# Kernel tuning notes

Measured on AMD Instinct MI355X. Metric: run time of the kernel, lower is better.

The kernel has to match this reference:

```python
import jax, jax.numpy as jnp
import numpy as np

NUM_HEADS = 8
EPS = 1e-12  # torch F.normalize default eps


def setup_inputs() -> dict:
    key = jax.random.key(0)
    k0, k1, k2, k3 = jax.random.split(key, 4)
    b, c, d, h, w = 2, 64, 8, 128, 128
    x = jax.random.normal(k0, (b, c, d, h, w), dtype=jnp.float32)
    # 1x1x1 conv weights stored as [out, in]; depthwise 3x3x3 as [out, 1, kd, kh, kw]
    w_qkv = jax.random.normal(k1, (3 * c, c), dtype=jnp.float32) * 0.05
    w_dw = jax.random.normal(k2, (3 * c, 1, 3, 3, 3), dtype=jnp.float32) * 0.05
    temperature = jnp.ones((NUM_HEADS, 1, 1), dtype=jnp.float32)
    w_proj = jax.random.normal(k3, (c, c), dtype=jnp.float32) * 0.05
    return {"x": x, "w_qkv": w_qkv, "w_dw": w_dw, "temperature": temperature, "w_proj": w_proj}


def _l2norm(t):
    # F.normalize(t, dim=-1): t / max(||t||, eps)
    n = jnp.sqrt(jnp.sum(t * t, axis=-1, keepdims=True))
    return t / jnp.maximum(n, EPS)


def reference(x, w_qkv, w_dw, temperature, w_proj):
    b, c, d, h, w = x.shape
    heads = NUM_HEADS
    ch = c // heads  # per-head channel dim
    # 1x1x1 conv (pointwise) -> einsum over channels
    qkv = jnp.einsum('bcdhw,oc->bodhw', x, w_qkv)
    # depthwise 3x3x3 conv, padding 1 (SAME), groups = 3*c
    qkv = jax.lax.conv_general_dilated(
        qkv, w_dw, window_strides=(1, 1, 1), padding=[(1, 1)] * 3,
        feature_group_count=3 * c,
        dimension_numbers=('NCDHW', 'OIDHW', 'NCDHW'))
    q, k, v = jnp.split(qkv, 3, axis=1)
    n = d * h * w
    q = q.reshape(b, heads, ch, n)
    k = k.reshape(b, heads, ch, n)
    v = v.reshape(b, heads, ch, n)
    q = _l2norm(q)
    k = _l2norm(k)
    # channel-channel attention: [b, heads, ch, ch]
    attn = jnp.einsum('bhcn,bhen->bhce', q, k) * temperature
    attn = jax.nn.softmax(attn, axis=-1)
    out = jnp.einsum('bhce,bhen->bhcn', attn, v)
    out = out.reshape(b, c, d, h, w)
    out = jnp.einsum('bcdhw,oc->bodhw', out, w_proj)
    return out
```

## Files before the change

### kernel.cpp

```cpp
#include <hip/hip_runtime.h>
#include <math.h>

#define NPOS 131072
#define GC 128

typedef __attribute__((ext_vector_type(8))) short short8v;
typedef __attribute__((ext_vector_type(4))) float f32x4;

__device__ __forceinline__ void bf16split(float x, unsigned short& hi, unsigned short& lo) {
  unsigned u = __float_as_uint(x);
  hi = (unsigned short)(u >> 16);
  float hif = __uint_as_float(u & 0xffff0000u);
  float l = x - hif;
  lo = (unsigned short)(__float_as_uint(l) >> 16);
}

__global__ void k_prep(const float* __restrict__ w_qkv, unsigned short* __restrict__ whi,
                       unsigned short* __restrict__ wlo) {
  int idx = blockIdx.x * 256 + threadIdx.x;
  if (idx < 12288) {
    int j = idx & 7, l = (idx >> 3) & 63, ks = (idx >> 9) & 1, ot = (idx >> 10) & 3,
        g = idx >> 12;
    int out = ot * 16 + (l & 15);
    int k = ks * 32 + (l >> 4) * 8 + j;
    bf16split(w_qkv[(g * 64 + out) * 64 + k], whi[idx], wlo[idx]);
  }
}

__global__ __launch_bounds__(256) void k_pw_mfma(const float* __restrict__ x,
                                                 const unsigned short* __restrict__ whi,
                                                 const unsigned short* __restrict__ wlo,
                                                 float* __restrict__ pre) {
  const int b = blockIdx.y;
  const int lane = threadIdx.x & 63;
  const int wid = threadIdx.x >> 6;
  const int p0 = blockIdx.x * 256 + wid * 64;
  short8v ahi[4][2], alo[4][2];
#pragma unroll
  for (int ot = 0; ot < 4; ++ot)
#pragma unroll
    for (int ks = 0; ks < 2; ++ks) {
      int fi = ((ot * 2 + ks) * 64 + lane) * 8;
      ahi[ot][ks] = *(const short8v*)&whi[fi];
      alo[ot][ks] = *(const short8v*)&wlo[fi];
    }
  const int prow = lane & 15, kgrp = lane >> 4;
  const float* xb = x + ((size_t)b * 64 + kgrp * 8) * NPOS;
#pragma unroll
  for (int pt = 0; pt < 4; ++pt) {
    const int p = p0 + pt * 16 + prow;
    float xv[16];
#pragma unroll
    for (int ks = 0; ks < 2; ++ks)
#pragma unroll
      for (int j = 0; j < 8; ++j)
        xv[ks * 8 + j] = xb[(size_t)(ks * 32 + j) * NPOS + p];
    short8v bh[2], bl[2];
#pragma unroll
    for (int ks = 0; ks < 2; ++ks)
#pragma unroll
      for (int j = 0; j < 8; ++j) {
        unsigned short h, lo16;
        bf16split(xv[ks * 8 + j], h, lo16);
        bh[ks][j] = (short)h;
        bl[ks][j] = (short)lo16;
      }
#pragma unroll
    for (int ot = 0; ot < 4; ++ot) {
      f32x4 D = {0.f, 0.f, 0.f, 0.f};
#pragma unroll
      for (int ks = 0; ks < 2; ++ks) {
        D = __builtin_amdgcn_mfma_f32_16x16x32_bf16(ahi[ot][ks], bh[ks], D, 0, 0, 0);
        D = __builtin_amdgcn_mfma_f32_16x16x32_bf16(ahi[ot][ks], bl[ks], D, 0, 0, 0);
        D = __builtin_amdgcn_mfma_f32_16x16x32_bf16(alo[ot][ks], bh[ks], D, 0, 0, 0);
      }
      float* ob = pre + ((size_t)b * 64 + ot * 16 + kgrp * 4) * NPOS + p;
#pragma unroll
      for (int jj = 0; jj < 4; ++jj) ob[(size_t)jj * NPOS] = D[jj];
    }
  }
}

__device__ __forceinline__ void stage_tile(float (*t)[10][40], const float* __restrict__ in,
                                           int h0, int w0, int tid) {
  for (int i = tid; i < 800; i += 256) {
    int j = i & 7, row = i >> 3;
    int h = row % 10, dpl = row / 10;
    int dd = dpl - 1, hh = h0 + h - 1;
    float4 v = make_float4(0.f, 0.f, 0.f, 0.f);
    if (dd >= 0 && dd < 8 && hh >= 0 && hh < 128)
      v = *(const float4*)&in[((size_t)dd * 128 + hh) * 128 + (w0 + j * 4)];
    *(float4*)&t[dpl][h][4 + j * 4] = v;
  }
  for (int i = tid; i < 200; i += 256) {
    int side = i & 1, row = i >> 1;
    int h = row % 10, dpl = row / 10;
    int dd = dpl - 1, hh = h0 + h - 1;
    int ww = side ? (w0 + 32) : (w0 - 1);
    float v = 0.f;
    if (dd >= 0 && dd < 8 && hh >= 0 && hh < 128 && ww >= 0 && ww < 128)
      v = in[((size_t)dd * 128 + hh) * 128 + ww];
    t[dpl][h][side ? 36 : 3] = v;
  }
}

__device__ __forceinline__ void conv_droll(const float (*t)[10][40], const float* wk,
                                           int hl, int wl, float* acc) {
#pragma unroll
  for (int d = 0; d < 8; ++d) acc[d] = 0.f;
#pragma unroll
  for (int dpl = 0; dpl < 10; ++dpl) {
#pragma unroll
    for (int kh = 0; kh < 3; ++kh) {
#pragma unroll
      for (int kw = 0; kw < 3; ++kw) {
        float f = t[dpl][hl + kh][3 + wl + kw];
#pragma unroll
        for (int kd = 0; kd < 3; ++kd) {
          const int d = dpl - kd;
          if (d >= 0 && d < 8)
            acc[d] = fmaf(f, wk[(kd * 3 + kh) * 3 + kw], acc[d]);
        }
      }
    }
  }
}

__global__ __launch_bounds__(256) void k_dw(const float* __restrict__ pre,
                                            const float* __restrict__ w_dw,
                                            float* __restrict__ conv,
                                            float* __restrict__ nsq, int g) {
  const int id = blockIdx.x;
  const int sid = (id & 7) * 1024 + (id >> 3);
  const int z = sid >> 6, r = sid & 63, by = r >> 2, bx = r & 3;
  const int b = z >> 6;
  const int c = z & 63;
  const int h0 = by * 8;
  const int w0 = bx * 32;
  __shared__ float t[10][10][40];
  __shared__ float red[4];
  const int tid = threadIdx.y * 32 + threadIdx.x;
  stage_tile(t, pre + ((size_t)b * 64 + c) * NPOS, h0, w0, tid);
  float wk[27];
#pragma unroll
  for (int i = 0; i < 27; ++i) wk[i] = w_dw[(g * 64 + c) * 27 + i];
  __syncthreads();
  const int wl = threadIdx.x, hl = threadIdx.y;
  float acc[8];
  conv_droll(t, wk, hl, wl, acc);
  float* outp = conv + ((size_t)b * 64 + c) * NPOS + (size_t)(h0 + hl) * 128 + (w0 + wl);
  float nsum = 0.f;
#pragma unroll
  for (int d = 0; d < 8; ++d) {
    outp[(size_t)d * 16384] = acc[d];
    nsum = fmaf(acc[d], acc[d], nsum);
  }
  if (nsq) {
    const int lane = tid & 63, wv = tid >> 6;
    float v = nsum;
    v += __shfl_down(v, 32); v += __shfl_down(v, 16); v += __shfl_down(v, 8);
    v += __shfl_down(v, 4);  v += __shfl_down(v, 2);  v += __shfl_down(v, 1);
    if (lane == 0) red[wv] = v;
    __syncthreads();
    if (tid == 0) {
      const int blk = by * 4 + bx;
      nsq[((size_t)b * 64 + c) * 64 + blk] = red[0] + red[1] + red[2] + red[3];
    }
  }
}

__global__ __launch_bounds__(256) void k_gramS(const float* __restrict__ qconv,
                                               const float* __restrict__ kconv,
                                               float* __restrict__ partialS) {
  const int chunk = blockIdx.x;
  const int bh = blockIdx.y;
  const int b = bh >> 3, head = bh & 7;
  const int tid = threadIdx.x;
  const size_t base = ((size_t)b * 64 + head * 8) * NPOS + (size_t)chunk * 1024 + tid;
  const float* qb = qconv + base;
  const float* kb = kconv + base;
  float S[64];
#pragma unroll
  for (int i = 0; i < 64; ++i) S[i] = 0.f;
#pragma unroll
  for (int it = 0; it < 4; ++it) {
    const size_t off = (size_t)it * 256;
    float qv[8], kv[8];
#pragma unroll
    for (int c = 0; c < 8; ++c) qv[c] = qb[(size_t)c * NPOS + off];
#pragma unroll
    for (int e = 0; e < 8; ++e) kv[e] = kb[(size_t)e * NPOS + off];
#pragma unroll
    for (int c = 0; c < 8; ++c)
#pragma unroll
      for (int e = 0; e < 8; ++e) S[c * 8 + e] = fmaf(qv[c], kv[e], S[c * 8 + e]);
  }
#pragma unroll
  for (int i = 0; i < 64; ++i) asm volatile("" : "+v"(S[i]));

  const int lane = tid & 63, wv = tid >> 6;
#define BSTEP(src, dst, n, s)                                        \
  {                                                                  \
    const bool hi_ = (lane >> (s)) & 1;                              \
    _Pragma("unroll")                                                \
    for (int i_ = 0; i_ < (n); ++i_) {                               \
      float send_ = hi_ ? src[i_] : src[i_ + (n)];                   \
      float mine_ = hi_ ? src[i_ + (n)] : src[i_];                   \
      dst[i_] = mine_ + __shfl_xor(send_, 1 << (s));                 \
    }                                                                \
  }
  float v32[32], v16[16], v8[8], v4[4], v2[2], v1[1];
  BSTEP(S,   v32, 32, 0)
  BSTEP(v32, v16, 16, 1)
  BSTEP(v16, v8,   8, 2)
  BSTEP(v8,  v4,   4, 3)
  BSTEP(v4,  v2,   2, 4)
  BSTEP(v2,  v1,   1, 5)
#undef BSTEP
  const int idx = ((lane & 1) << 5) | ((lane & 2) << 3) | ((lane & 4) << 1) |
                  ((lane & 8) >> 1) | ((lane & 16) >> 3) | ((lane & 32) >> 5);
  __shared__ float red[4][64];
  red[wv][idx] = v1[0];
  __syncthreads();
  if (tid < 64) {
    float s = red[0][tid] + red[1][tid] + red[2][tid] + red[3][tid];
    partialS[((size_t)bh * GC + chunk) * 64 + tid] = s;
  }
}

__global__ void k_attn(const float* __restrict__ partialS, const float* __restrict__ nqp,
                       const float* __restrict__ nkp, const float* __restrict__ temp,
                       float* __restrict__ A) {
  const int bh = blockIdx.x;
  const int b = bh >> 3, head = bh & 7;
  const int tid = threadIdx.x;
  __shared__ float sums[80];
  if (tid < 64) {
    float s = 0.f;
    const float* pp = partialS + (size_t)bh * GC * 64 + tid;
    for (int j = 0; j < GC; ++j) s += pp[j * 64];
    sums[tid] = s;
  } else if (tid < 72) {
    const int e = tid - 64;
    float s = 0.f;
    const float* pp = nkp + ((size_t)b * 64 + head * 8 + e) * 64;
    for (int j = 0; j < 64; ++j) s += pp[j];
    sums[64 + e] = s;
  } else if (tid < 80) {
    const int c = tid - 72;
    float s = 0.f;
    const float* pp = nqp + ((size_t)b * 64 + head * 8 + c) * 64;
    for (int j = 0; j < 64; ++j) s += pp[j];
    sums[72 + c] = s;
  }
  __syncthreads();
  if (tid < 8) {
    const int c = tid;
    float tp = temp[head];
    float qd = fmaxf(sqrtf(sums[72 + c]), 1e-12f);
    float vals[8];
    float mx = -1e30f;
#pragma unroll
    for (int e = 0; e < 8; ++e) {
      float kd = fmaxf(sqrtf(sums[64 + e]), 1e-12f);
      vals[e] = sums[c * 8 + e] / (qd * kd) * tp;
      mx = fmaxf(mx, vals[e]);
    }
    float den = 0.f;
#pragma unroll
    for (int e = 0; e < 8; ++e) { vals[e] = expf(vals[e] - mx); den += vals[e]; }
#pragma unroll
    for (int e = 0; e < 8; ++e) A[bh * 64 + c * 8 + e] = vals[e] / den;
  }
}

__global__ void k_M(const float* __restrict__ w_proj, const float* __restrict__ A,
                    unsigned short* __restrict__ Mhi, unsigned short* __restrict__ Mlo) {
  const int b = blockIdx.x;
  for (int e = threadIdx.x; e < 4096; e += 256) {
    int j = e & 7, l = (e >> 3) & 63, ks = (e >> 9) & 1, ot = (e >> 10) & 3;
    int out = ot * 16 + (l & 15);
    int gch = ks * 32 + (l >> 4) * 8 + j;
    int hg = gch >> 3, jj = gch & 7;
    float s = 0.f;
#pragma unroll
    for (int i = 0; i < 8; ++i)
      s += w_proj[out * 64 + hg * 8 + i] * A[(b * 8 + hg) * 64 + i * 8 + jj];
    bf16split(s, Mhi[b * 4096 + e], Mlo[b * 4096 + e]);
  }
}

__global__ __launch_bounds__(256) void k_out_mfma(const float* __restrict__ vconv,
                                                  const unsigned short* __restrict__ Mhi,
                                                  const unsigned short* __restrict__ Mlo,
                                                  float* __restrict__ out) {
  const int b = blockIdx.y;
  const int lane = threadIdx.x & 63;
  const int wid = threadIdx.x >> 6;
  const int p0 = blockIdx.x * 256 + wid * 64;
  short8v ahi[4][2], alo[4][2];
#pragma unroll
  for (int ot = 0; ot < 4; ++ot)
#pragma unroll
    for (int ks = 0; ks < 2; ++ks) {
      int fi = b * 4096 + ((ot * 2 + ks) * 64 + lane) * 8;
      ahi[ot][ks] = *(const short8v*)&Mhi[fi];
      alo[ot][ks] = *(const short8v*)&Mlo[fi];
    }
  const int prow = lane & 15, kgrp = lane >> 4;
  const float* vb = vconv + ((size_t)b * 64 + kgrp * 8) * NPOS;
#pragma unroll
  for (int pt = 0; pt < 4; ++pt) {
    const int p = p0 + pt * 16 + prow;
    float xv[16];
#pragma unroll
    for (int ks = 0; ks < 2; ++ks)
#pragma unroll
      for (int j = 0; j < 8; ++j)
        xv[ks * 8 + j] = vb[(size_t)(ks * 32 + j) * NPOS + p];
    short8v bh[2], bl[2];
#pragma unroll
    for (int ks = 0; ks < 2; ++ks)
#pragma unroll
      for (int j = 0; j < 8; ++j) {
        unsigned short h, lo16;
        bf16split(xv[ks * 8 + j], h, lo16);
        bh[ks][j] = (short)h;
        bl[ks][j] = (short)lo16;
      }
#pragma unroll
    for (int ot = 0; ot < 4; ++ot) {
      f32x4 D = {0.f, 0.f, 0.f, 0.f};
#pragma unroll
      for (int ks = 0; ks < 2; ++ks) {
        D = __builtin_amdgcn_mfma_f32_16x16x32_bf16(ahi[ot][ks], bh[ks], D, 0, 0, 0);
        D = __builtin_amdgcn_mfma_f32_16x16x32_bf16(ahi[ot][ks], bl[ks], D, 0, 0, 0);
        D = __builtin_amdgcn_mfma_f32_16x16x32_bf16(alo[ot][ks], bh[ks], D, 0, 0, 0);
      }
      float* ob = out + ((size_t)b * 64 + ot * 16 + kgrp * 4) * NPOS + p;
#pragma unroll
      for (int jj = 0; jj < 4; ++jj) ob[(size_t)jj * NPOS] = D[jj];
    }
  }
}

extern "C" void kernel_launch(void* const* d_in, const int* in_sizes, int n_in,
                              void* d_out, int out_size, void* d_ws, size_t ws_size,
                              hipStream_t stream) {
  const float* x      = (const float*)d_in[0];
  const float* w_qkv  = (const float*)d_in[1];
  const float* w_dw   = (const float*)d_in[2];
  const float* temp   = (const float*)d_in[3];
  const float* w_proj = (const float*)d_in[4];
  float* out = (float*)d_out;
  float* ws  = (float*)d_ws;

  float* conv_buf = ws;
  float* kconv    = conv_buf + 16777216ull;
  float* nqp      = kconv + 16777216ull;
  float* nkp      = nqp + 8192ull;
  float* partialS = nkp + 8192ull;
  float* Abuf     = partialS + 131072ull;
  unsigned short* whi = (unsigned short*)(Abuf + 1024ull);
  unsigned short* wlo = whi + 12288ull;
  unsigned short* Mhi = wlo + 12288ull;
  unsigned short* Mlo = Mhi + 8192ull;

  k_prep<<<48, 256, 0, stream>>>(w_qkv, whi, wlo);
  k_pw_mfma<<<dim3(512, 2), 256, 0, stream>>>(x, whi, wlo, out);
  k_dw<<<8192, dim3(32, 8), 0, stream>>>(out, w_dw, conv_buf, nqp, 0);
  k_pw_mfma<<<dim3(512, 2), 256, 0, stream>>>(x, whi + 4096, wlo + 4096, out);
  k_dw<<<8192, dim3(32, 8), 0, stream>>>(out, w_dw, kconv, nkp, 1);
  k_gramS<<<dim3(GC, 16), 256, 0, stream>>>(conv_buf, kconv, partialS);
  k_attn<<<16, 128, 0, stream>>>(partialS, nqp, nkp, temp, Abuf);
  k_M<<<2, 256, 0, stream>>>(w_proj, Abuf, Mhi, Mlo);
  k_pw_mfma<<<dim3(512, 2), 256, 0, stream>>>(x, whi + 8192, wlo + 8192, out);
  k_dw<<<8192, dim3(32, 8), 0, stream>>>(out, w_dw, conv_buf, nullptr, 2);
  k_out_mfma<<<dim3(512, 2), 256, 0, stream>>>(conv_buf, Mhi, Mlo, out);
}
```

Measured before the change: 235.1 us.

## Stage pointwise-conv input tiles in LDS and split output channels across waves

The pointwise MFMA kernels now load a 64-channel by 64-position input tile into shared memory with coalesced float4 reads. Each of the four waves then computes one 16-row output-channel tile instead of all four. The old version had each wave read its own positions with strided scalar loads. The grid grows fourfold to match. This reduces per-wave weight registers and improves load coalescing, at the cost of a block barrier and LDS traffic with possible bank conflicts on the column reads.

```diff
diff --git a/kernel.cpp b/kernel.cpp
--- a/kernel.cpp
+++ b/kernel.cpp
@@ -33,51 +33,53 @@
                                                  float* __restrict__ pre) {
   const int b = blockIdx.y;
   const int lane = threadIdx.x & 63;
-  const int wid = threadIdx.x >> 6;
-  const int p0 = blockIdx.x * 256 + wid * 64;
-  short8v ahi[4][2], alo[4][2];
-#pragma unroll
-  for (int ot = 0; ot < 4; ++ot)
-#pragma unroll
-    for (int ks = 0; ks < 2; ++ks) {
-      int fi = ((ot * 2 + ks) * 64 + lane) * 8;
-      ahi[ot][ks] = *(const short8v*)&whi[fi];
-      alo[ot][ks] = *(const short8v*)&wlo[fi];
-    }
+  const int ot = threadIdx.x >> 6;
+  const int p0 = blockIdx.x * 64;
+  __shared__ float xl[64][66];
+  short8v ahi[2], alo[2];
+#pragma unroll
+  for (int ks = 0; ks < 2; ++ks) {
+    int fi = ((ot * 2 + ks) * 64 + lane) * 8;
+    ahi[ks] = *(const short8v*)&whi[fi];
+    alo[ks] = *(const short8v*)&wlo[fi];
+  }
+  const float* xb = x + ((size_t)b * 64) * NPOS + p0;
+  const int tid = threadIdx.x;
+#pragma unroll
+  for (int r = 0; r < 4; ++r) {
+    int idx = r * 256 + tid;
+    int ch = idx >> 4, f4 = idx & 15;
+    float4 g = *(const float4*)&xb[(size_t)ch * NPOS + f4 * 4];
+    xl[ch][f4 * 4 + 0] = g.x;
+    xl[ch][f4 * 4 + 1] = g.y;
+    xl[ch][f4 * 4 + 2] = g.z;
+    xl[ch][f4 * 4 + 3] = g.w;
+  }
+  __syncthreads();
   const int prow = lane & 15, kgrp = lane >> 4;
-  const float* xb = x + ((size_t)b * 64 + kgrp * 8) * NPOS;
 #pragma unroll
   for (int pt = 0; pt < 4; ++pt) {
-    const int p = p0 + pt * 16 + prow;
-    float xv[16];
-#pragma unroll
-    for (int ks = 0; ks < 2; ++ks)
-#pragma unroll
-      for (int j = 0; j < 8; ++j)
-        xv[ks * 8 + j] = xb[(size_t)(ks * 32 + j) * NPOS + p];
+    const int pos = pt * 16 + prow;
     short8v bh[2], bl[2];
 #pragma unroll
     for (int ks = 0; ks < 2; ++ks)
 #pragma unroll
       for (int j = 0; j < 8; ++j) {
         unsigned short h, lo16;
-        bf16split(xv[ks * 8 + j], h, lo16);
+        bf16split(xl[ks * 32 + kgrp * 8 + j][pos], h, lo16);
         bh[ks][j] = (short)h;
         bl[ks][j] = (short)lo16;
       }
-#pragma unroll
-    for (int ot = 0; ot < 4; ++ot) {
-      f32x4 D = {0.f, 0.f, 0.f, 0.f};
-#pragma unroll
-      for (int ks = 0; ks < 2; ++ks) {
-        D = __builtin_amdgcn_mfma_f32_16x16x32_bf16(ahi[ot][ks], bh[ks], D, 0, 0, 0);
-        D = __builtin_amdgcn_mfma_f32_16x16x32_bf16(ahi[ot][ks], bl[ks], D, 0, 0, 0);
-        D = __builtin_amdgcn_mfma_f32_16x16x32_bf16(alo[ot][ks], bh[ks], D, 0, 0, 0);
-      }
-      float* ob = pre + ((size_t)b * 64 + ot * 16 + kgrp * 4) * NPOS + p;
-#pragma unroll
-      for (int jj = 0; jj < 4; ++jj) ob[(size_t)jj * NPOS] = D[jj];
-    }
+    f32x4 D = {0.f, 0.f, 0.f, 0.f};
+#pragma unroll
+    for (int ks = 0; ks < 2; ++ks) {
+      D = __builtin_amdgcn_mfma_f32_16x16x32_bf16(ahi[ks], bh[ks], D, 0, 0, 0);
+      D = __builtin_amdgcn_mfma_f32_16x16x32_bf16(ahi[ks], bl[ks], D, 0, 0, 0);
+      D = __builtin_amdgcn_mfma_f32_16x16x32_bf16(alo[ks], bh[ks], D, 0, 0, 0);
+    }
+    float* ob = pre + ((size_t)b * 64 + ot * 16 + kgrp * 4) * NPOS + p0 + pos;
+#pragma unroll
+    for (int jj = 0; jj < 4; ++jj) ob[(size_t)jj * NPOS] = D[jj];
   }
 }
 
@@ -296,51 +298,53 @@
                                                   float* __restrict__ out) {
   const int b = blockIdx.y;
   const int lane = threadIdx.x & 63;
-  const int wid = threadIdx.x >> 6;
-  const int p0 = blockIdx.x * 256 + wid * 64;
-  short8v ahi[4][2], alo[4][2];
-#pragma unroll
-  for (int ot = 0; ot < 4; ++ot)
-#pragma unroll
-    for (int ks = 0; ks < 2; ++ks) {
-      int fi = b * 4096 + ((ot * 2 + ks) * 64 + lane) * 8;
-      ahi[ot][ks] = *(const short8v*)&Mhi[fi];
-      alo[ot][ks] = *(const short8v*)&Mlo[fi];
-    }
+  const int ot = threadIdx.x >> 6;
+  const int p0 = blockIdx.x * 64;
+  __shared__ float xl[64][66];
+  short8v ahi[2], alo[2];
+#pragma unroll
+  for (int ks = 0; ks < 2; ++ks) {
+    int fi = b * 4096 + ((ot * 2 + ks) * 64 + lane) * 8;
+    ahi[ks] = *(const short8v*)&Mhi[fi];
+    alo[ks] = *(const short8v*)&Mlo[fi];
+  }
+  const float* vb = vconv + ((size_t)b * 64) * NPOS + p0;
+  const int tid = threadIdx.x;
+#pragma unroll
+  for (int r = 0; r < 4; ++r) {
+    int idx = r * 256 + tid;
+    int ch = idx >> 4, f4 = idx & 15;
+    float4 g = *(const float4*)&vb[(size_t)ch * NPOS + f4 * 4];
+    xl[ch][f4 * 4 + 0] = g.x;
+    xl[ch][f4 * 4 + 1] = g.y;
+    xl[ch][f4 * 4 + 2] = g.z;
+    xl[ch][f4 * 4 + 3] = g.w;
+  }
+  __syncthreads();
   const int prow = lane & 15, kgrp = lane >> 4;
-  const float* vb = vconv + ((size_t)b * 64 + kgrp * 8) * NPOS;
 #pragma unroll
   for (int pt = 0; pt < 4; ++pt) {
-    const int p = p0 + pt * 16 + prow;
-    float xv[16];
-#pragma unroll
-    for (int ks = 0; ks < 2; ++ks)
-#pragma unroll
-      for (int j = 0; j < 8; ++j)
-        xv[ks * 8 + j] = vb[(size_t)(ks * 32 + j) * NPOS + p];
+    const int pos = pt * 16 + prow;
     short8v bh[2], bl[2];
 #pragma unroll
     for (int ks = 0; ks < 2; ++ks)
 #pragma unroll
       for (int j = 0; j < 8; ++j) {
         unsigned short h, lo16;
-        bf16split(xv[ks * 8 + j], h, lo16);
+        bf16split(xl[ks * 32 + kgrp * 8 + j][pos], h, lo16);
         bh[ks][j] = (short)h;
         bl[ks][j] = (short)lo16;
       }
-#pragma unroll
-    for (int ot = 0; ot < 4; ++ot) {
-      f32x4 D = {0.f, 0.f, 0.f, 0.f};
-#pragma unroll
-      for (int ks = 0; ks < 2; ++ks) {
-        D = __builtin_amdgcn_mfma_f32_16x16x32_bf16(ahi[ot][ks], bh[ks], D, 0, 0, 0);
-        D = __builtin_amdgcn_mfma_f32_16x16x32_bf16(ahi[ot][ks], bl[ks], D, 0, 0, 0);
-        D = __builtin_amdgcn_mfma_f32_16x16x32_bf16(alo[ot][ks], bh[ks], D, 0, 0, 0);
-      }
-      float* ob = out + ((size_t)b * 64 + ot * 16 + kgrp * 4) * NPOS + p;
-#pragma unroll
-      for (int jj = 0; jj < 4; ++jj) ob[(size_t)jj * NPOS] = D[jj];
-    }
+    f32x4 D = {0.f, 0.f, 0.f, 0.f};
+#pragma unroll
+    for (int ks = 0; ks < 2; ++ks) {
+      D = __builtin_amdgcn_mfma_f32_16x16x32_bf16(ahi[ks], bh[ks], D, 0, 0, 0);
+      D = __builtin_amdgcn_mfma_f32_16x16x32_bf16(ahi[ks], bl[ks], D, 0, 0, 0);
+      D = __builtin_amdgcn_mfma_f32_16x16x32_bf16(alo[ks], bh[ks], D, 0, 0, 0);
+    }
+    float* ob = out + ((size_t)b * 64 + ot * 16 + kgrp * 4) * NPOS + p0 + pos;
+#pragma unroll
+    for (int jj = 0; jj < 4; ++jj) ob[(size_t)jj * NPOS] = D[jj];
   }
 }
 
@@ -367,14 +371,14 @@
   unsigned short* Mlo = Mhi + 8192ull;
 
   k_prep<<<48, 256, 0, stream>>>(w_qkv, whi, wlo);
-  k_pw_mfma<<<dim3(512, 2), 256, 0, stream>>>(x, whi, wlo, out);
+  k_pw_mfma<<<dim3(2048, 2), 256, 0, stream>>>(x, whi, wlo, out);
   k_dw<<<8192, dim3(32, 8), 0, stream>>>(out, w_dw, conv_buf, nqp, 0);
-  k_pw_mfma<<<dim3(512, 2), 256, 0, stream>>>(x, whi + 4096, wlo + 4096, out);
+  k_pw_mfma<<<dim3(2048, 2), 256, 0, stream>>>(x, whi + 4096, wlo + 4096, out);
   k_dw<<<8192, dim3(32, 8), 0, stream>>>(out, w_dw, kconv, nkp, 1);
   k_gramS<<<dim3(GC, 16), 256, 0, stream>>>(conv_buf, kconv, partialS);
   k_attn<<<16, 128, 0, stream>>>(partialS, nqp, nkp, temp, Abuf);
   k_M<<<2, 256, 0, stream>>>(w_proj, Abuf, Mhi, Mlo);
-  k_pw_mfma<<<dim3(512, 2), 256, 0, stream>>>(x, whi + 8192, wlo + 8192, out);
+  k_pw_mfma<<<dim3(2048, 2), 256, 0, stream>>>(x, whi + 8192, wlo + 8192, out);
   k_dw<<<8192, dim3(32, 8), 0, stream>>>(out, w_dw, conv_buf, nullptr, 2);
-  k_out_mfma<<<dim3(512, 2), 256, 0, stream>>>(conv_buf, Mhi, Mlo, out);
-}
+  k_out_mfma<<<dim3(2048, 2), 256, 0, stream>>>(conv_buf, Mhi, Mlo, out);
+}
```

Measured after the change: 222.4 us. -5.4%, faster.
